# Kernel tuning notes

Measured on AMD Instinct MI355X. Metric: run time of the kernel, lower is better.

Reference implementation:

```python
import jax, jax.numpy as jnp
import numpy as np

NUM_RBF = 16
TOP_K = 30
LOWER = 0.0
UPPER = 20.0
MAX_REL = 32  # PositionalEncodings max_relative_feature


def layer_norm(x, g, b, eps=1e-5):
    m = jnp.mean(x, -1, keepdims=True)
    v = jnp.var(x, -1, keepdims=True)
    return (x - m) / jnp.sqrt(v + eps) * g + b


def rbf(D):
    # exp(-((D - mu)/sigma)^2), mu = linspace(LOWER, UPPER, NUM_RBF)
    mu = jnp.linspace(LOWER, UPPER, NUM_RBF)
    sigma = (UPPER - LOWER) / NUM_RBF
    return jnp.exp(-(((D[..., None] - mu) / sigma) ** 2))


def setup_inputs() -> dict:
    key = jax.random.key(0)
    ks = jax.random.split(key, 6)
    B, L, A = 1, 1536, 14
    x = jax.random.normal(ks[0], (B, L, A, 3), jnp.float32) * 5.0
    S = jax.random.randint(ks[1], (B, L), 0, 21)
    mask = jnp.ones((B, L), jnp.float32)
    atom14_mask = jnp.ones((B, L, A), jnp.float32)
    R_idx = jnp.broadcast_to(jnp.arange(L, dtype=jnp.int32), (B, L))
    chain_labels = jnp.zeros((B, L), jnp.int32)
    protein_mpnn_feat = jax.random.normal(ks[2], (B, L, 128), jnp.float32)
    W_pos = jax.random.normal(ks[3], (2 * MAX_REL + 2, 16), jnp.float32) * 0.12
    b_pos = jnp.zeros((16,), jnp.float32)
    W_edge = jax.random.normal(ks[4], (16 + NUM_RBF * 14 * 14, 128), jnp.float32) * 0.018
    gamma_e = jnp.ones((128,), jnp.float32)
    beta_e = jnp.zeros((128,), jnp.float32)
    W_node = jax.random.normal(ks[5], (21 + 128, 128), jnp.float32) * 0.08
    gamma_n = jnp.ones((128,), jnp.float32)
    beta_n = jnp.zeros((128,), jnp.float32)
    return dict(x=x, mask=mask, atom14_mask=atom14_mask,
                protein_mpnn_feat=protein_mpnn_feat,
                W_pos=W_pos, b_pos=b_pos, W_edge=W_edge, gamma_e=gamma_e,
                beta_e=beta_e, W_node=W_node, gamma_n=gamma_n, beta_n=beta_n,
                S=S, R_idx=R_idx, chain_labels=chain_labels)


def reference(x, mask, atom14_mask, protein_mpnn_feat,
              W_pos, b_pos, W_edge, gamma_e, beta_e,
              W_node, gamma_n, beta_n, S, R_idx, chain_labels):
    B, L, A, _ = x.shape  # A = 14
    X_m = atom14_mask * mask[:, :, None]          # [B,L,14]
    Ca = x[:, :, 1]                                # CA_idx = 1

    # ---- _dist: masked pairwise CA distances + kNN topk (smallest) ----
    m2 = mask[:, None, :] * mask[:, :, None]       # [B,L,L]
    dX = Ca[:, None, :, :] - Ca[:, :, None, :]
    D = m2 * jnp.sqrt(jnp.sum(dX ** 2, -1) + 1e-6)
    D_max = jnp.max(D, -1, keepdims=True)
    D_adjust = D + (1.0 - m2) * D_max
    _, E_idx = jax.lax.top_k(-D_adjust, TOP_K)     # [B,L,K] smallest distances

    bidx = jnp.arange(B)[:, None, None]
    # gather neighbor atom coords / masks (all_coords_list == x in atom14 order)
    Xg = x[bidx, E_idx]                            # [B,L,K,14,3]
    Xm_g = X_m[bidx, E_idx]                        # [B,L,K,14]

    # ---- 14x14 pairwise atom RBFs to neighbors, fused/vectorized ----
    # Dp[b,l,k,i,j] = ||x[b,l,i] - x[b,E_idx[b,l,k],j]||
    Dp = jnp.sqrt(jnp.sum((x[:, :, None, :, None, :] - Xg[:, :, :, None, :, :]) ** 2, -1) + 1e-6)
    R = rbf(Dp)                                    # [B,L,K,14,14,16]
    R = R * X_m[:, :, None, :, None, None] * Xm_g[:, :, :, None, :, None]
    # torch loop cats atom_1-major, atom_2, then rbf bins -> same as reshape
    RBF_all = R.reshape(B, L, TOP_K, A * A * NUM_RBF)  # [B,L,K,3136]

    # ---- positional encodings ----
    offset = R_idx[:, :, None] - R_idx[:, None, :]           # [B,L,L]
    offset_g = jnp.take_along_axis(offset, E_idx, axis=2)    # [B,L,K]
    d_chains = (chain_labels[:, :, None] == chain_labels[:, None, :]).astype(jnp.int32)
    E_chains = jnp.take_along_axis(d_chains, E_idx, axis=2)  # [B,L,K]
    d = jnp.clip(offset_g + MAX_REL, 0, 2 * MAX_REL) * E_chains \
        + (1 - E_chains) * (2 * MAX_REL + 1)
    E_pos = jax.nn.one_hot(d, 2 * MAX_REL + 2, dtype=x.dtype) @ W_pos + b_pos

    # ---- edge embedding ----
    E = jnp.concatenate([E_pos, RBF_all], -1) @ W_edge       # [B,L,K,128]
    E = layer_norm(E, gamma_e, beta_e)

    # ---- node embedding ----
    V = jnp.concatenate([jax.nn.one_hot(S, 21, dtype=x.dtype), protein_mpnn_feat], -1) @ W_node
    V = layer_norm(V, gamma_n, beta_n)

    return (V, E, E_idx, x)
```

## Files before the change

### kernel.cpp

```cpp
#include <hip/hip_runtime.h>
#include <hip/hip_bf16.h>
#include <hip/hip_fp16.h>
#include <math.h>

#define LL 1536
#define NA 14
#define TOPK 30
#define KDIM 3152
#define KPAD 3200
#define NCHUNK 50

#define TOPK_BLKS 384
#define CONV_BLKS 100
#define NODE_BLKS 384
#define PREP_BLKS (TOPK_BLKS + CONV_BLKS + NODE_BLKS)

#define EDGE_BLKS 768

typedef __attribute__((ext_vector_type(8))) short bf16x8;
typedef __attribute__((ext_vector_type(4))) float f32x4;

static __device__ __forceinline__ float fexp2(float f) {
    return __builtin_amdgcn_exp2f(f);
}

static __device__ __forceinline__ unsigned cvt_pk_bf16(float lo, float hi) {
    unsigned r;
    asm("v_cvt_pk_bf16_f32 %0, %1, %2" : "=v"(r) : "v"(lo), "v"(hi));
    return r;
}

static __device__ __forceinline__ unsigned long long u64min(
    unsigned long long a, unsigned long long b) { return a < b ? a : b; }

#define ASYNC16(ldsp, gp)                                                     \
    __builtin_amdgcn_global_load_lds(                                         \
        (const __attribute__((address_space(1))) void*)(gp),                  \
        (__attribute__((address_space(3))) void*)(ldsp), 16, 0, 0)

static __device__ __forceinline__ void build_rbf(
    ushort* dst, float4 xi4, float4 xj4,
    const float (&cA)[7], const float (&cB)[7])
{
    float dx = xi4.x - xj4.x, dy = xi4.y - xj4.y, dz = xi4.z - xj4.z;
    float dd = sqrtf(dx * dx + dy * dy + dz * dz + 1e-6f);
    dd = fminf(dd, 27.f);
    float coef = xi4.w * xj4.w;
    float w = fexp2(dd * 2.46219921f);
    float ev[16];
    float s8 = dd - 10.66666667f;
    ev[0] = fexp2(-0.92332483f * dd * dd) * coef;
    ev[8] = fexp2(-0.92332483f * s8 * s8) * coef;
    #pragma unroll
    for (int j = 1; j <= 7; ++j) {
        ev[j]     = ev[j - 1]     * w * cA[j - 1];
        ev[8 + j] = ev[8 + j - 1] * w * cB[j - 1];
    }
    union { unsigned u[8]; uint4 q[2]; } o;
    #pragma unroll
    for (int c = 0; c < 8; ++c) o.u[c] = cvt_pk_bf16(ev[2 * c], ev[2 * c + 1]);
    *(uint4*)&dst[0] = o.q[0];
    *(uint4*)&dst[8] = o.q[1];
}

__global__ __launch_bounds__(256) void prep_kernel(
    const float* __restrict__ x, const float* __restrict__ mask,
    const float* __restrict__ feat,
    const float* __restrict__ W_edge, ushort* __restrict__ Wt,
    const float* __restrict__ W_node, const float* __restrict__ gamma_n,
    const float* __restrict__ beta_n, const int* __restrict__ S,
    float* __restrict__ V, float* __restrict__ out_idx, float* __restrict__ out_x)
{
    __shared__ __align__(16) char sm[24576];
    const int blk = blockIdx.x;
    const int tid = threadIdx.x;

    if (blk < TOPK_BLKS) {
        float* ca  = (float*)sm;
        float* msk = (float*)sm + 4608;
        for (int t = tid; t < LL; t += 256) {
            msk[t] = mask[t];
            ca[t * 3 + 0] = x[t * 42 + 3];
            ca[t * 3 + 1] = x[t * 42 + 4];
            ca[t * 3 + 2] = x[t * 42 + 5];
        }
        __syncthreads();

        const int lane = tid & 63;
        const int i = blk * 4 + (tid >> 6);
        const float cix = ca[i * 3 + 0], ciy = ca[i * 3 + 1], ciz = ca[i * 3 + 2];
        const float mi = msk[i];

        float d[24], m2a[24];
        float lmax = 0.f;
        #pragma unroll
        for (int c = 0; c < 24; ++c) {
            int j = lane + c * 64;
            float dx = ca[j * 3 + 0] - cix;
            float dy = ca[j * 3 + 1] - ciy;
            float dz = ca[j * 3 + 2] - ciz;
            float m2 = mi * msk[j];
            float D = m2 * sqrtf(dx * dx + dy * dy + dz * dz + 1e-6f);
            d[c] = D; m2a[c] = m2;
            lmax = fmaxf(lmax, D);
        }
        #pragma unroll
        for (int m = 1; m < 64; m <<= 1) lmax = fmaxf(lmax, __shfl_xor(lmax, m));

        unsigned long long key[24];
        #pragma unroll
        for (int c = 0; c < 24; ++c) {
            float adj = d[c] + (1.f - m2a[c]) * lmax;
            key[c] = ((unsigned long long)__float_as_uint(adj) << 32)
                   | (unsigned)(lane + c * 64);
        }
        for (int t = 0; t < TOPK; ++t) {
            unsigned long long m12[12];
            #pragma unroll
            for (int c = 0; c < 12; ++c) m12[c] = u64min(key[2 * c], key[2 * c + 1]);
            #pragma unroll
            for (int c = 0; c < 6; ++c) m12[c] = u64min(m12[2 * c], m12[2 * c + 1]);
            unsigned long long best = u64min(u64min(m12[0], m12[1]),
                u64min(m12[2], u64min(m12[3], u64min(m12[4], m12[5]))));
            #pragma unroll
            for (int m = 1; m < 64; m <<= 1) best = u64min(best, __shfl_xor(best, m));
            if (lane == 0) out_idx[i * TOPK + t] = (float)(unsigned)(best & 0xffffffffu);
            #pragma unroll
            for (int c = 0; c < 24; ++c) if (key[c] == best) key[c] = ~0ull;
        }
        for (int t = lane; t < 42; t += 64) out_x[i * 42 + t] = x[i * 42 + t];

    } else if (blk < TOPK_BLKS + CONV_BLKS) {
        int cb = blk - TOPK_BLKS;
        int k0 = (cb % 50) * 64, n0 = (cb / 50) * 64;
        float (*tile)[65] = (float (*)[65])sm;
        #pragma unroll
        for (int r = 0; r < 16; ++r) {
            int idx = r * 256 + tid;
            int kl = idx >> 6, nl = idx & 63;
            int k = k0 + kl;
            tile[nl][kl] = (k < KDIM) ? W_edge[k * 128 + n0 + nl] : 0.f;
        }
        __syncthreads();
        #pragma unroll
        for (int r = 0; r < 8; ++r) {
            int idx = r * 256 + tid;
            int nl = idx >> 5, kp = (idx & 31) * 2;
            unsigned pk = cvt_pk_bf16(tile[nl][kp], tile[nl][kp + 1]);
            *(unsigned*)&Wt[(size_t)(n0 + nl) * KPAD + k0 + kp] = pk;
        }

    } else {
        int nb = blk - TOPK_BLKS - CONV_BLKS;
        float* f = (float*)sm;
        const int w = tid >> 6, lane = tid & 63;
        const int i = nb * 4 + w;
        f[w * 128 + lane] = feat[i * 128 + lane];
        f[w * 128 + 64 + lane] = feat[i * 128 + 64 + lane];
        __syncthreads();
        int s = S[i];
        float a0 = W_node[s * 128 + lane];
        float a1 = W_node[s * 128 + 64 + lane];
        #pragma unroll 8
        for (int c = 0; c < 128; ++c) {
            float fc = f[w * 128 + c];
            a0 = fmaf(fc, W_node[(21 + c) * 128 + lane], a0);
            a1 = fmaf(fc, W_node[(21 + c) * 128 + 64 + lane], a1);
        }
        float ss = a0 + a1, qq = a0 * a0 + a1 * a1;
        #pragma unroll
        for (int m = 1; m < 64; m <<= 1) {
            ss += __shfl_xor(ss, m);
            qq += __shfl_xor(qq, m);
        }
        float mean = ss * (1.f / 128.f);
        float var = qq * (1.f / 128.f) - mean * mean;
        float inv = 1.f / sqrtf(var + 1e-5f);
        V[i * 128 + lane]      = (a0 - mean) * inv * gamma_n[lane] + beta_n[lane];
        V[i * 128 + 64 + lane] = (a1 - mean) * inv * gamma_n[64 + lane] + beta_n[64 + lane];
    }
}

__global__ __launch_bounds__(256, 3) void edge_mfma_kernel(
    const float* __restrict__ x, const float* __restrict__ mask,
    const float* __restrict__ a14m, const float* __restrict__ W_pos,
    const float* __restrict__ b_pos, const ushort* __restrict__ Wt,
    const float* __restrict__ gamma, const float* __restrict__ beta,
    const int* __restrict__ R_idx, const int* __restrict__ chain,
    const float* __restrict__ idxf, float* __restrict__ E)
{
    __shared__ __align__(16) ushort Bs[128 * 64];
    __shared__ __align__(16) ushort As[64 * 72];
    __shared__ __align__(16) float4 xjr[64][14];
    __shared__ __align__(16) float4 xir[2][14];
    __shared__ int   jl[64];
    __shared__ float lnS[64][2];
    __shared__ float lnQ[64][2];

    const int i0 = blockIdx.x * 2;
    const int tid = threadIdx.x;
    const int wave = tid >> 6, lane = tid & 63;

    if (tid < 64) {
        int g = tid >> 5, e = tid & 31;
        jl[tid] = (e < TOPK) ? (int)idxf[(i0 + g) * TOPK + e] : 0;
    } else if (tid < 64 + 28) {
        int t = tid - 64, g = t / 14, a = t - g * 14;
        const float* xp = &x[(i0 + g) * 42 + a * 3];
        xir[g][a] = make_float4(xp[0], xp[1], xp[2],
                                a14m[(i0 + g) * 14 + a] * mask[i0 + g]);
    }
    __syncthreads();

    for (int t = tid; t < 64 * 14; t += 256) {
        int row = t / 14, a = t - row * 14;
        int e = row & 31, j = jl[row];
        const float* xp = &x[j * 42 + a * 3];
        float mj = (e < TOPK) ? a14m[j * 14 + a] * mask[j] : 0.f;
        xjr[row][a] = make_float4(xp[0], xp[1], xp[2], mj);
    }
    __syncthreads();

    const int l16 = lane & 15, lk = lane >> 4, lk8 = lk * 8;
    const int mh = wave >> 1, nh = wave & 1;
    const int arow0 = (mh * 32 + l16) * 72, arow1 = arow0 + 16 * 72;
    const int row_b = tid >> 2, slot = tid & 3;
    const int gb = row_b >> 5, eb = row_b & 31;
    ushort* bdst = &As[row_b * 72 + slot * 16];

    float cA[7], cB[7];
    #pragma unroll
    for (int j = 1; j <= 7; ++j) {
        cA[j - 1] = __expf(-1.13777778f * (float)(2 * j - 1));
        cB[j - 1] = __expf(-1.13777778f * (float)(2 * (j + 8) - 1));
    }

    const int srow = wave * 32 + (lane >> 3);
    const int sseg = (lane & 7) ^ ((lane >> 3) & 7);
    const ushort* gsrc = Wt + (size_t)srow * KPAD + sseg * 8;

    #pragma unroll
    for (int it = 0; it < 4; ++it)
        ASYNC16(Bs + wave * 2048 + it * 512, gsrc + (size_t)it * 8 * KPAD);

    if (slot == 0) {
        float v[16];
        if (eb < TOPK) {
            int i = i0 + gb, j = jl[row_b];
            int off = R_idx[i] - R_idx[j];
            int ec = (chain[i] == chain[j]) ? 1 : 0;
            int dc = off + 32; dc = dc < 0 ? 0 : (dc > 64 ? 64 : dc);
            int d = ec ? dc : 65;
            #pragma unroll
            for (int c = 0; c < 16; ++c) v[c] = W_pos[d * 16 + c] + b_pos[c];
        } else {
            #pragma unroll
            for (int c = 0; c < 16; ++c) v[c] = 0.f;
        }
        union { unsigned u[8]; uint4 q[2]; } o;
        #pragma unroll
        for (int c = 0; c < 8; ++c) o.u[c] = cvt_pk_bf16(v[2 * c], v[2 * c + 1]);
        *(uint4*)&bdst[0] = o.q[0];
        *(uint4*)&bdst[8] = o.q[1];
    } else {
        build_rbf(bdst, xir[gb][0], xjr[row_b][slot - 1], cA, cB);
    }

    int boff[2][4];
    #pragma unroll
    for (int ks = 0; ks < 2; ++ks)
        #pragma unroll
        for (int nf = 0; nf < 4; ++nf) {
            int n = nh * 64 + nf * 16 + l16;
            boff[ks][nf] = n * 64 + ((((ks << 2) | lk) ^ (n & 7)) << 3);
        }

    int p = slot + 3, a1 = 0, a2 = slot + 3;
    f32x4 acc[2][4] = {};

    __syncthreads();

    for (int ch = 0; ch < NCHUNK; ++ch) {
        bf16x8 afr[2][2], bfr[2][4];
        #pragma unroll
        for (int ks = 0; ks < 2; ++ks) {
            afr[ks][0] = *(const bf16x8*)&As[arow0 + ks * 32 + lk8];
            afr[ks][1] = *(const bf16x8*)&As[arow1 + ks * 32 + lk8];
            #pragma unroll
            for (int nf = 0; nf < 4; ++nf)
                bfr[ks][nf] = *(const bf16x8*)&Bs[boff[ks][nf]];
        }
        __syncthreads();

        if (ch + 1 < NCHUNK) {
            #pragma unroll
            for (int it = 0; it < 4; ++it)
                ASYNC16(Bs + wave * 2048 + it * 512,
                        gsrc + (size_t)it * 8 * KPAD + (ch + 1) * 64);
            if (p <= 195) {
                build_rbf(bdst, xir[gb][a1], xjr[row_b][a2], cA, cB);
            } else {
                uint4 z = {0u, 0u, 0u, 0u};
                *(uint4*)&bdst[0] = z;
                *(uint4*)&bdst[8] = z;
            }
            p += 4; a2 += 4; if (a2 >= 14) { a2 -= 14; ++a1; }
        }

        #pragma unroll
        for (int ks = 0; ks < 2; ++ks)
            #pragma unroll
            for (int mf = 0; mf < 2; ++mf)
                #pragma unroll
                for (int nf = 0; nf < 4; ++nf)
                    acc[mf][nf] = __builtin_amdgcn_mfma_f32_16x16x32_bf16(
                        afr[ks][mf], bfr[ks][nf], acc[mf][nf], 0, 0, 0);

        __syncthreads();
    }

    #pragma unroll
    for (int mf = 0; mf < 2; ++mf)
        #pragma unroll
        for (int reg = 0; reg < 4; ++reg) {
            float s = acc[mf][0][reg] + acc[mf][1][reg] + acc[mf][2][reg] + acc[mf][3][reg];
            float q = acc[mf][0][reg] * acc[mf][0][reg] + acc[mf][1][reg] * acc[mf][1][reg]
                    + acc[mf][2][reg] * acc[mf][2][reg] + acc[mf][3][reg] * acc[mf][3][reg];
            #pragma unroll
            for (int m = 1; m < 16; m <<= 1) {
                s += __shfl_xor(s, m);
                q += __shfl_xor(q, m);
            }
            if (l16 == 0) {
                int row = mh * 32 + mf * 16 + lk * 4 + reg;
                lnS[row][nh] = s;
                lnQ[row][nh] = q;
            }
        }
    __syncthreads();

    float gl[4], bl[4];
    #pragma unroll
    for (int nf = 0; nf < 4; ++nf) {
        int col = nh * 64 + nf * 16 + l16;
        gl[nf] = gamma[col];
        bl[nf] = beta[col];
    }
    #pragma unroll
    for (int mf = 0; mf < 2; ++mf)
        #pragma unroll
        for (int reg = 0; reg < 4; ++reg) {
            int r = mh * 32 + mf * 16 + lk * 4 + reg;
            int e = r & 31, g = r >> 5;
            if (e < TOPK) {
                float s = lnS[r][0] + lnS[r][1];
                float q = lnQ[r][0] + lnQ[r][1];
                float mean = s * (1.f / 128.f);
                float var = q * (1.f / 128.f) - mean * mean;
                float inv = 1.f / sqrtf(var + 1e-5f);
                float* dst = &E[((size_t)((i0 + g) * TOPK + e)) * 128];
                #pragma unroll
                for (int nf = 0; nf < 4; ++nf) {
                    int col = nh * 64 + nf * 16 + l16;
                    dst[col] = (acc[mf][nf][reg] - mean) * inv * gl[nf] + bl[nf];
                }
            }
        }
}

extern "C" void kernel_launch(void* const* d_in, const int* in_sizes, int n_in,
                              void* d_out, int out_size, void* d_ws, size_t ws_size,
                              hipStream_t stream)
{
    const float* x       = (const float*)d_in[0];
    const float* mask    = (const float*)d_in[1];
    const float* a14m    = (const float*)d_in[2];
    const float* feat    = (const float*)d_in[3];
    const float* W_pos   = (const float*)d_in[4];
    const float* b_pos   = (const float*)d_in[5];
    const float* W_edge  = (const float*)d_in[6];
    const float* gamma_e = (const float*)d_in[7];
    const float* beta_e  = (const float*)d_in[8];
    const float* W_node  = (const float*)d_in[9];
    const float* gamma_n = (const float*)d_in[10];
    const float* beta_n  = (const float*)d_in[11];
    const int*   S       = (const int*)d_in[12];
    const int*   R_idx   = (const int*)d_in[13];
    const int*   chain   = (const int*)d_in[14];

    float* out     = (float*)d_out;
    float* V       = out;
    float* E       = out + 196608;
    float* out_idx = out + 196608 + 5898240;
    float* out_x   = out_idx + 46080;

    ushort* Wt = (ushort*)d_ws;

    prep_kernel<<<PREP_BLKS, 256, 0, stream>>>(
        x, mask, feat, W_edge, Wt, W_node, gamma_n, beta_n, S, V, out_idx, out_x);
    edge_mfma_kernel<<<EDGE_BLKS, 256, 0, stream>>>(
        x, mask, a14m, W_pos, b_pos, Wt, gamma_e, beta_e, R_idx, chain,
        out_idx, E);
}
```

Measured before the change: 101.5 us.

## Fuse top-k and node embedding into edge MFMA kernel, store neighbor coords as fp16

Moves the kNN top-k selection and node layer-norm embedding into the edge GEMM kernel. Each block computes top-k for its own two residues in two waves while the other two waves compute the node embedding. The selected indices go straight to LDS, so the global round-trip of indices and one launch boundary are removed. Weight conversion stays as a small separate kernel. Neighbor atom coordinates are kept in LDS as fp16 to shrink the shared footprint. Each block now redundantly loads all CA coordinates and leaves the MFMA waves idle during top-k. The fp16 coordinates can lose accuracy on distances.

Measured after the change: 104.5 us. 1.03x slower.

```diff
diff --git a/kernel.cpp b/kernel.cpp
--- a/kernel.cpp
+++ b/kernel.cpp
@@ -10,12 +10,7 @@
 #define KPAD 3200
 #define NCHUNK 50
 
-#define TOPK_BLKS 384
-#define CONV_BLKS 100
-#define NODE_BLKS 384
-#define PREP_BLKS (TOPK_BLKS + CONV_BLKS + NODE_BLKS)
-
-#define EDGE_BLKS 768
+#define MAIN_BLKS 768
 
 typedef __attribute__((ext_vector_type(8))) short bf16x8;
 typedef __attribute__((ext_vector_type(4))) float f32x4;
@@ -39,13 +34,14 @@
         (__attribute__((address_space(3))) void*)(ldsp), 16, 0, 0)
 
 static __device__ __forceinline__ void build_rbf(
-    ushort* dst, float4 xi4, float4 xj4,
+    ushort* dst, float xix, float xiy, float xiz, float mi_,
+    float xjx, float xjy, float xjz, float mj_,
     const float (&cA)[7], const float (&cB)[7])
 {
-    float dx = xi4.x - xj4.x, dy = xi4.y - xj4.y, dz = xi4.z - xj4.z;
+    float dx = xix - xjx, dy = xiy - xjy, dz = xiz - xjz;
     float dd = sqrtf(dx * dx + dy * dy + dz * dz + 1e-6f);
     dd = fminf(dd, 27.f);
-    float coef = xi4.w * xj4.w;
+    float coef = mi_ * mj_;
     float w = fexp2(dd * 2.46219921f);
     float ev[16];
     float s8 = dd - 10.66666667f;
@@ -63,31 +59,72 @@
     *(uint4*)&dst[8] = o.q[1];
 }
 
-__global__ __launch_bounds__(256) void prep_kernel(
+__global__ __launch_bounds__(256) void conv_kernel(
+    const float* __restrict__ W_edge, ushort* __restrict__ Wt)
+{
+    __shared__ float tile[64][65];
+    const int k0 = blockIdx.x * 64, n0 = blockIdx.y * 64;
+    const int tid = threadIdx.x;
+    #pragma unroll
+    for (int r = 0; r < 16; ++r) {
+        int idx = r * 256 + tid;
+        int kl = idx >> 6, nl = idx & 63;
+        int k = k0 + kl;
+        tile[nl][kl] = (k < KDIM) ? W_edge[k * 128 + n0 + nl] : 0.f;
+    }
+    __syncthreads();
+    #pragma unroll
+    for (int r = 0; r < 8; ++r) {
+        int idx = r * 256 + tid;
+        int nl = idx >> 5, kp = (idx & 31) * 2;
+        unsigned pk = cvt_pk_bf16(tile[nl][kp], tile[nl][kp + 1]);
+        *(unsigned*)&Wt[(size_t)(n0 + nl) * KPAD + k0 + kp] = pk;
+    }
+}
+
+__global__ __launch_bounds__(256, 3) void main_kernel(
     const float* __restrict__ x, const float* __restrict__ mask,
-    const float* __restrict__ feat,
-    const float* __restrict__ W_edge, ushort* __restrict__ Wt,
-    const float* __restrict__ W_node, const float* __restrict__ gamma_n,
-    const float* __restrict__ beta_n, const int* __restrict__ S,
-    float* __restrict__ V, float* __restrict__ out_idx, float* __restrict__ out_x)
+    const float* __restrict__ a14m, const float* __restrict__ W_pos,
+    const float* __restrict__ b_pos, const ushort* __restrict__ Wt,
+    const float* __restrict__ gamma, const float* __restrict__ beta,
+    const int* __restrict__ R_idx, const int* __restrict__ chain,
+    const float* __restrict__ feat, const float* __restrict__ W_node,
+    const float* __restrict__ gamma_n, const float* __restrict__ beta_n,
+    const int* __restrict__ S,
+    float* __restrict__ V, float* __restrict__ E,
+    float* __restrict__ out_idx, float* __restrict__ out_x)
 {
-    __shared__ __align__(16) char sm[24576];
-    const int blk = blockIdx.x;
+    __shared__ __align__(16) char arena[34496];
+    ushort* Bs  = (ushort*)arena;
+    ushort* As  = (ushort*)(arena + 16384);
+    __half* xjh = (__half*)(arena + 25600);
+    float4* xir = (float4*)(arena + 32768);
+    int*    jl  = (int*)(arena + 33216);
+    float*  lnS = (float*)(arena + 33472);
+    float*  lnQ = (float*)(arena + 33984);
+    float* ca   = (float*)arena;
+    float* msk  = (float*)(arena + 18432);
+    float* fbuf = (float*)(arena + 25600);
+
+    const int i0 = blockIdx.x * 2;
     const int tid = threadIdx.x;
-
-    if (blk < TOPK_BLKS) {
-        float* ca  = (float*)sm;
-        float* msk = (float*)sm + 4608;
-        for (int t = tid; t < LL; t += 256) {
-            msk[t] = mask[t];
-            ca[t * 3 + 0] = x[t * 42 + 3];
-            ca[t * 3 + 1] = x[t * 42 + 4];
-            ca[t * 3 + 2] = x[t * 42 + 5];
-        }
-        __syncthreads();
-
-        const int lane = tid & 63;
-        const int i = blk * 4 + (tid >> 6);
+    const int wave = tid >> 6, lane = tid & 63;
+
+    for (int t = tid; t < LL; t += 256) {
+        msk[t] = mask[t];
+        ca[t * 3 + 0] = x[t * 42 + 3];
+        ca[t * 3 + 1] = x[t * 42 + 4];
+        ca[t * 3 + 2] = x[t * 42 + 5];
+    }
+    if (wave >= 2) {
+        int i = i0 + wave - 2;
+        fbuf[(wave - 2) * 128 + lane] = feat[i * 128 + lane];
+        fbuf[(wave - 2) * 128 + 64 + lane] = feat[i * 128 + 64 + lane];
+    }
+    __syncthreads();
+
+    if (wave < 2) {
+        const int i = i0 + wave;
         const float cix = ca[i * 3 + 0], ciy = ca[i * 3 + 1], ciz = ca[i * 3 + 2];
         const float mi = msk[i];
 
@@ -124,46 +161,24 @@
                 u64min(m12[2], u64min(m12[3], u64min(m12[4], m12[5]))));
             #pragma unroll
             for (int m = 1; m < 64; m <<= 1) best = u64min(best, __shfl_xor(best, m));
-            if (lane == 0) out_idx[i * TOPK + t] = (float)(unsigned)(best & 0xffffffffu);
+            int j = (int)(best & 0xffffffffu);
+            if (lane == 0) {
+                out_idx[i * TOPK + t] = (float)j;
+                jl[wave * 32 + t] = j;
+            }
             #pragma unroll
             for (int c = 0; c < 24; ++c) if (key[c] == best) key[c] = ~0ull;
         }
-        for (int t = lane; t < 42; t += 64) out_x[i * 42 + t] = x[i * 42 + t];
-
-    } else if (blk < TOPK_BLKS + CONV_BLKS) {
-        int cb = blk - TOPK_BLKS;
-        int k0 = (cb % 50) * 64, n0 = (cb / 50) * 64;
-        float (*tile)[65] = (float (*)[65])sm;
-        #pragma unroll
-        for (int r = 0; r < 16; ++r) {
-            int idx = r * 256 + tid;
-            int kl = idx >> 6, nl = idx & 63;
-            int k = k0 + kl;
-            tile[nl][kl] = (k < KDIM) ? W_edge[k * 128 + n0 + nl] : 0.f;
-        }
-        __syncthreads();
-        #pragma unroll
-        for (int r = 0; r < 8; ++r) {
-            int idx = r * 256 + tid;
-            int nl = idx >> 5, kp = (idx & 31) * 2;
-            unsigned pk = cvt_pk_bf16(tile[nl][kp], tile[nl][kp + 1]);
-            *(unsigned*)&Wt[(size_t)(n0 + nl) * KPAD + k0 + kp] = pk;
-        }
-
+        if (lane >= TOPK && lane < 32) jl[wave * 32 + lane] = 0;
     } else {
-        int nb = blk - TOPK_BLKS - CONV_BLKS;
-        float* f = (float*)sm;
-        const int w = tid >> 6, lane = tid & 63;
-        const int i = nb * 4 + w;
-        f[w * 128 + lane] = feat[i * 128 + lane];
-        f[w * 128 + 64 + lane] = feat[i * 128 + 64 + lane];
-        __syncthreads();
+        const int w2 = wave - 2;
+        const int i = i0 + w2;
         int s = S[i];
         float a0 = W_node[s * 128 + lane];
         float a1 = W_node[s * 128 + 64 + lane];
         #pragma unroll 8
         for (int c = 0; c < 128; ++c) {
-            float fc = f[w * 128 + c];
+            float fc = fbuf[w2 * 128 + c];
             a0 = fmaf(fc, W_node[(21 + c) * 128 + lane], a0);
             a1 = fmaf(fc, W_node[(21 + c) * 128 + 64 + lane], a1);
         }
@@ -178,46 +193,34 @@
         float inv = 1.f / sqrtf(var + 1e-5f);
         V[i * 128 + lane]      = (a0 - mean) * inv * gamma_n[lane] + beta_n[lane];
         V[i * 128 + 64 + lane] = (a1 - mean) * inv * gamma_n[64 + lane] + beta_n[64 + lane];
-    }
-}
-
-__global__ __launch_bounds__(256, 3) void edge_mfma_kernel(
-    const float* __restrict__ x, const float* __restrict__ mask,
-    const float* __restrict__ a14m, const float* __restrict__ W_pos,
-    const float* __restrict__ b_pos, const ushort* __restrict__ Wt,
-    const float* __restrict__ gamma, const float* __restrict__ beta,
-    const int* __restrict__ R_idx, const int* __restrict__ chain,
-    const float* __restrict__ idxf, float* __restrict__ E)
-{
-    __shared__ __align__(16) ushort Bs[128 * 64];
-    __shared__ __align__(16) ushort As[64 * 72];
-    __shared__ __align__(16) float4 xjr[64][14];
-    __shared__ __align__(16) float4 xir[2][14];
-    __shared__ int   jl[64];
-    __shared__ float lnS[64][2];
-    __shared__ float lnQ[64][2];
-
-    const int i0 = blockIdx.x * 2;
-    const int tid = threadIdx.x;
-    const int wave = tid >> 6, lane = tid & 63;
-
-    if (tid < 64) {
-        int g = tid >> 5, e = tid & 31;
-        jl[tid] = (e < TOPK) ? (int)idxf[(i0 + g) * TOPK + e] : 0;
-    } else if (tid < 64 + 28) {
-        int t = tid - 64, g = t / 14, a = t - g * 14;
+        for (int t = lane; t < 42; t += 64) out_x[i * 42 + t] = x[i * 42 + t];
+    }
+    __syncthreads();
+
+    const int srow = wave * 32 + (lane >> 3);
+    const int sseg = (lane & 7) ^ ((lane >> 3) & 7);
+    const ushort* gsrc = Wt + (size_t)srow * KPAD + sseg * 8;
+    #pragma unroll
+    for (int it = 0; it < 4; ++it)
+        ASYNC16(Bs + wave * 2048 + it * 512, gsrc + (size_t)it * 8 * KPAD);
+
+    if (tid < 28) {
+        int g = tid / 14, a = tid - g * 14;
         const float* xp = &x[(i0 + g) * 42 + a * 3];
-        xir[g][a] = make_float4(xp[0], xp[1], xp[2],
-                                a14m[(i0 + g) * 14 + a] * mask[i0 + g]);
-    }
-    __syncthreads();
-
+        xir[g * 14 + a] = make_float4(xp[0], xp[1], xp[2],
+                                      a14m[(i0 + g) * 14 + a] * mask[i0 + g]);
+    }
     for (int t = tid; t < 64 * 14; t += 256) {
         int row = t / 14, a = t - row * 14;
         int e = row & 31, j = jl[row];
         const float* xp = &x[j * 42 + a * 3];
         float mj = (e < TOPK) ? a14m[j * 14 + a] * mask[j] : 0.f;
-        xjr[row][a] = make_float4(xp[0], xp[1], xp[2], mj);
+        union { __half h[4]; short4 s4; } u;
+        u.h[0] = __float2half(xp[0]);
+        u.h[1] = __float2half(xp[1]);
+        u.h[2] = __float2half(xp[2]);
+        u.h[3] = __float2half(mj);
+        *(short4*)&xjh[t * 4] = u.s4;
     }
     __syncthreads();
 
@@ -234,14 +237,6 @@
         cA[j - 1] = __expf(-1.13777778f * (float)(2 * j - 1));
         cB[j - 1] = __expf(-1.13777778f * (float)(2 * (j + 8) - 1));
     }
-
-    const int srow = wave * 32 + (lane >> 3);
-    const int sseg = (lane & 7) ^ ((lane >> 3) & 7);
-    const ushort* gsrc = Wt + (size_t)srow * KPAD + sseg * 8;
-
-    #pragma unroll
-    for (int it = 0; it < 4; ++it)
-        ASYNC16(Bs + wave * 2048 + it * 512, gsrc + (size_t)it * 8 * KPAD);
 
     if (slot == 0) {
         float v[16];
@@ -263,7 +258,12 @@
         *(uint4*)&bdst[0] = o.q[0];
         *(uint4*)&bdst[8] = o.q[1];
     } else {
-        build_rbf(bdst, xir[gb][0], xjr[row_b][slot - 1], cA, cB);
+        float4 xi4 = xir[gb * 14 + 0];
+        union { __half h[4]; short4 s4; } u;
+        u.s4 = *(const short4*)&xjh[(row_b * 14 + slot - 1) * 4];
+        build_rbf(bdst, xi4.x, xi4.y, xi4.z, xi4.w,
+                  __half2float(u.h[0]), __half2float(u.h[1]),
+                  __half2float(u.h[2]), __half2float(u.h[3]), cA, cB);
     }
 
     int boff[2][4];
@@ -275,7 +275,7 @@
             boff[ks][nf] = n * 64 + ((((ks << 2) | lk) ^ (n & 7)) << 3);
         }
 
-    int p = slot + 3, a1 = 0, a2 = slot + 3;
+    int p = slot + 3, a1i = 0, a2i = slot + 3;
     f32x4 acc[2][4] = {};
 
     __syncthreads();
@@ -298,13 +298,18 @@
                 ASYNC16(Bs + wave * 2048 + it * 512,
                         gsrc + (size_t)it * 8 * KPAD + (ch + 1) * 64);
             if (p <= 195) {
-                build_rbf(bdst, xir[gb][a1], xjr[row_b][a2], cA, cB);
+                float4 xi4 = xir[gb * 14 + a1i];
+                union { __half h[4]; short4 s4; } u;
+                u.s4 = *(const short4*)&xjh[(row_b * 14 + a2i) * 4];
+                build_rbf(bdst, xi4.x, xi4.y, xi4.z, xi4.w,
+                          __half2float(u.h[0]), __half2float(u.h[1]),
+                          __half2float(u.h[2]), __half2float(u.h[3]), cA, cB);
             } else {
                 uint4 z = {0u, 0u, 0u, 0u};
                 *(uint4*)&bdst[0] = z;
                 *(uint4*)&bdst[8] = z;
             }
-            p += 4; a2 += 4; if (a2 >= 14) { a2 -= 14; ++a1; }
+            p += 4; a2i += 4; if (a2i >= 14) { a2i -= 14; ++a1i; }
         }
 
         #pragma unroll
@@ -333,8 +338,8 @@
             }
             if (l16 == 0) {
                 int row = mh * 32 + mf * 16 + lk * 4 + reg;
-                lnS[row][nh] = s;
-                lnQ[row][nh] = q;
+                lnS[row * 2 + nh] = s;
+                lnQ[row * 2 + nh] = q;
             }
         }
     __syncthreads();
@@ -353,8 +358,8 @@
             int r = mh * 32 + mf * 16 + lk * 4 + reg;
             int e = r & 31, g = r >> 5;
             if (e < TOPK) {
-                float s = lnS[r][0] + lnS[r][1];
-                float q = lnQ[r][0] + lnQ[r][1];
+                float s = lnS[r * 2 + 0] + lnS[r * 2 + 1];
+                float q = lnQ[r * 2 + 0] + lnQ[r * 2 + 1];
                 float mean = s * (1.f / 128.f);
                 float var = q * (1.f / 128.f) - mean * mean;
                 float inv = 1.f / sqrtf(var + 1e-5f);
@@ -396,9 +401,8 @@
 
     ushort* Wt = (ushort*)d_ws;
 
-    prep_kernel<<<PREP_BLKS, 256, 0, stream>>>(
-        x, mask, feat, W_edge, Wt, W_node, gamma_n, beta_n, S, V, out_idx, out_x);
-    edge_mfma_kernel<<<EDGE_BLKS, 256, 0, stream>>>(
+    conv_kernel<<<dim3(50, 2), 256, 0, stream>>>(W_edge, Wt);
+    main_kernel<<<MAIN_BLKS, 256, 0, stream>>>(
         x, mask, a14m, W_pos, b_pos, Wt, gamma_e, beta_e, R_idx, chain,
-        out_idx, E);
-}
+        feat, W_node, gamma_n, beta_n, S, V, E, out_idx, out_x);
+}
```

## Move node embedding and x copy into edge kernel epilogue, raise MFMA priority

Applied to the files above, without the earlier changes.

Removes the node-embedding blocks and the x passthrough copy from the prep kernel and computes them in the epilogue of the edge MFMA kernel. Each edge block handles the two residues it already owns, with an LDS reduction across waves for the layer norm. The goal is to shorten the serial prep kernel that gates the edge kernel. It also wraps the MFMA loop in s_setprio to favour matrix issue. The cost is a longer edge-kernel tail: a 128-step scalar loop per thread reading feat and W_node directly from global memory, plus two extra barriers.

Result: slower. 105.3 us (+3.7%).

```diff
diff --git a/kernel.cpp b/kernel.cpp
--- a/kernel.cpp
+++ b/kernel.cpp
@@ -12,8 +12,7 @@
 
 #define TOPK_BLKS 384
 #define CONV_BLKS 100
-#define NODE_BLKS 384
-#define PREP_BLKS (TOPK_BLKS + CONV_BLKS + NODE_BLKS)
+#define PREP_BLKS (TOPK_BLKS + CONV_BLKS)
 
 #define EDGE_BLKS 768
 
@@ -65,11 +64,8 @@
 
 __global__ __launch_bounds__(256) void prep_kernel(
     const float* __restrict__ x, const float* __restrict__ mask,
-    const float* __restrict__ feat,
     const float* __restrict__ W_edge, ushort* __restrict__ Wt,
-    const float* __restrict__ W_node, const float* __restrict__ gamma_n,
-    const float* __restrict__ beta_n, const int* __restrict__ S,
-    float* __restrict__ V, float* __restrict__ out_idx, float* __restrict__ out_x)
+    float* __restrict__ out_idx)
 {
     __shared__ __align__(16) char sm[24576];
     const int blk = blockIdx.x;
@@ -128,9 +124,8 @@
             #pragma unroll
             for (int c = 0; c < 24; ++c) if (key[c] == best) key[c] = ~0ull;
         }
-        for (int t = lane; t < 42; t += 64) out_x[i * 42 + t] = x[i * 42 + t];
-
-    } else if (blk < TOPK_BLKS + CONV_BLKS) {
+
+    } else {
         int cb = blk - TOPK_BLKS;
         int k0 = (cb % 50) * 64, n0 = (cb / 50) * 64;
         float (*tile)[65] = (float (*)[65])sm;
@@ -149,35 +144,6 @@
             unsigned pk = cvt_pk_bf16(tile[nl][kp], tile[nl][kp + 1]);
             *(unsigned*)&Wt[(size_t)(n0 + nl) * KPAD + k0 + kp] = pk;
         }
-
-    } else {
-        int nb = blk - TOPK_BLKS - CONV_BLKS;
-        float* f = (float*)sm;
-        const int w = tid >> 6, lane = tid & 63;
-        const int i = nb * 4 + w;
-        f[w * 128 + lane] = feat[i * 128 + lane];
-        f[w * 128 + 64 + lane] = feat[i * 128 + 64 + lane];
-        __syncthreads();
-        int s = S[i];
-        float a0 = W_node[s * 128 + lane];
-        float a1 = W_node[s * 128 + 64 + lane];
-        #pragma unroll 8
-        for (int c = 0; c < 128; ++c) {
-            float fc = f[w * 128 + c];
-            a0 = fmaf(fc, W_node[(21 + c) * 128 + lane], a0);
-            a1 = fmaf(fc, W_node[(21 + c) * 128 + 64 + lane], a1);
-        }
-        float ss = a0 + a1, qq = a0 * a0 + a1 * a1;
-        #pragma unroll
-        for (int m = 1; m < 64; m <<= 1) {
-            ss += __shfl_xor(ss, m);
-            qq += __shfl_xor(qq, m);
-        }
-        float mean = ss * (1.f / 128.f);
-        float var = qq * (1.f / 128.f) - mean * mean;
-        float inv = 1.f / sqrtf(var + 1e-5f);
-        V[i * 128 + lane]      = (a0 - mean) * inv * gamma_n[lane] + beta_n[lane];
-        V[i * 128 + 64 + lane] = (a1 - mean) * inv * gamma_n[64 + lane] + beta_n[64 + lane];
     }
 }
 
@@ -187,7 +153,11 @@
     const float* __restrict__ b_pos, const ushort* __restrict__ Wt,
     const float* __restrict__ gamma, const float* __restrict__ beta,
     const int* __restrict__ R_idx, const int* __restrict__ chain,
-    const float* __restrict__ idxf, float* __restrict__ E)
+    const float* __restrict__ idxf,
+    const float* __restrict__ feat, const float* __restrict__ W_node,
+    const float* __restrict__ gamma_n, const float* __restrict__ beta_n,
+    const int* __restrict__ S,
+    float* __restrict__ E, float* __restrict__ V, float* __restrict__ out_x)
 {
     __shared__ __align__(16) ushort Bs[128 * 64];
     __shared__ __align__(16) ushort As[64 * 72];
@@ -307,6 +277,7 @@
             p += 4; a2 += 4; if (a2 >= 14) { a2 -= 14; ++a1; }
         }
 
+        __builtin_amdgcn_s_setprio(1);
         #pragma unroll
         for (int ks = 0; ks < 2; ++ks)
             #pragma unroll
@@ -315,6 +286,7 @@
                 for (int nf = 0; nf < 4; ++nf)
                     acc[mf][nf] = __builtin_amdgcn_mfma_f32_16x16x32_bf16(
                         afr[ks][mf], bfr[ks][nf], acc[mf][nf], 0, 0, 0);
+        __builtin_amdgcn_s_setprio(0);
 
         __syncthreads();
     }
@@ -339,33 +311,62 @@
         }
     __syncthreads();
 
-    float gl[4], bl[4];
-    #pragma unroll
-    for (int nf = 0; nf < 4; ++nf) {
-        int col = nh * 64 + nf * 16 + l16;
-        gl[nf] = gamma[col];
-        bl[nf] = beta[col];
-    }
-    #pragma unroll
-    for (int mf = 0; mf < 2; ++mf)
-        #pragma unroll
-        for (int reg = 0; reg < 4; ++reg) {
-            int r = mh * 32 + mf * 16 + lk * 4 + reg;
-            int e = r & 31, g = r >> 5;
-            if (e < TOPK) {
-                float s = lnS[r][0] + lnS[r][1];
-                float q = lnQ[r][0] + lnQ[r][1];
-                float mean = s * (1.f / 128.f);
-                float var = q * (1.f / 128.f) - mean * mean;
-                float inv = 1.f / sqrtf(var + 1e-5f);
-                float* dst = &E[((size_t)((i0 + g) * TOPK + e)) * 128];
-                #pragma unroll
-                for (int nf = 0; nf < 4; ++nf) {
-                    int col = nh * 64 + nf * 16 + l16;
-                    dst[col] = (acc[mf][nf][reg] - mean) * inv * gl[nf] + bl[nf];
+    {
+        float gl[4], bl[4];
+        #pragma unroll
+        for (int nf = 0; nf < 4; ++nf) {
+            int col = nh * 64 + nf * 16 + l16;
+            gl[nf] = gamma[col];
+            bl[nf] = beta[col];
+        }
+        #pragma unroll
+        for (int mf = 0; mf < 2; ++mf)
+            #pragma unroll
+            for (int reg = 0; reg < 4; ++reg) {
+                int r = mh * 32 + mf * 16 + lk * 4 + reg;
+                int e = r & 31, g = r >> 5;
+                if (e < TOPK) {
+                    float s = lnS[r][0] + lnS[r][1];
+                    float q = lnQ[r][0] + lnQ[r][1];
+                    float mean = s * (1.f / 128.f);
+                    float var = q * (1.f / 128.f) - mean * mean;
+                    float inv = 1.f / sqrtf(var + 1e-5f);
+                    float* dst = &E[((size_t)((i0 + g) * TOPK + e)) * 128];
+                    #pragma unroll
+                    for (int nf = 0; nf < 4; ++nf) {
+                        int col = nh * 64 + nf * 16 + l16;
+                        dst[col] = (acc[mf][nf][reg] - mean) * inv * gl[nf] + bl[nf];
+                    }
                 }
             }
-        }
+    }
+
+    {
+        const int i = i0 + mh;
+        const int col = nh * 64 + lane;
+        int s = S[i];
+        float a = W_node[s * 128 + col];
+        #pragma unroll 8
+        for (int c = 0; c < 128; ++c)
+            a = fmaf(feat[i * 128 + c], W_node[(21 + c) * 128 + col], a);
+        float ss = a, qq = a * a;
+        #pragma unroll
+        for (int m = 1; m < 64; m <<= 1) {
+            ss += __shfl_xor(ss, m);
+            qq += __shfl_xor(qq, m);
+        }
+        __syncthreads();
+        if (lane == 0) { lnS[0][mh * 2 + nh] = ss; lnQ[0][mh * 2 + nh] = qq; }
+        __syncthreads();
+        float fss = lnS[0][mh * 2 + 0] + lnS[0][mh * 2 + 1];
+        float fqq = lnQ[0][mh * 2 + 0] + lnQ[0][mh * 2 + 1];
+        float mean = fss * (1.f / 128.f);
+        float var = fqq * (1.f / 128.f) - mean * mean;
+        float inv = 1.f / sqrtf(var + 1e-5f);
+        V[i * 128 + col] = (a - mean) * inv * gamma_n[col] + beta_n[col];
+
+        for (int t = tid; t < 84; t += 256) out_x[i0 * 42 + t] = x[i0 * 42 + t];
+    }
 }
 
 extern "C" void kernel_launch(void* const* d_in, const int* in_sizes, int n_in,
@@ -396,9 +397,8 @@
 
     ushort* Wt = (ushort*)d_ws;
 
-    prep_kernel<<<PREP_BLKS, 256, 0, stream>>>(
-        x, mask, feat, W_edge, Wt, W_node, gamma_n, beta_n, S, V, out_idx, out_x);
+    prep_kernel<<<PREP_BLKS, 256, 0, stream>>>(x, mask, W_edge, Wt, out_idx);
     edge_mfma_kernel<<<EDGE_BLKS, 256, 0, stream>>>(
         x, mask, a14m, W_pos, b_pos, Wt, gamma_e, beta_e, R_idx, chain,
-        out_idx, E);
-}
+        out_idx, feat, W_node, gamma_n, beta_n, S, E, V, out_x);
+}
```
